# Kernel tuning notes

Measured on AMD Instinct MI355X. Metric: run time of the kernel, lower is better.

## Reference

```python
import jax, jax.numpy as jnp
import numpy as np

N_ATOMS = 8192
N_PAIRS = 65536
F = 128        # n_atombasis
R = 20         # n_radialbasis
B = 5          # graph_n_blocks
EPS = 1e-8     # stability constant


def setup_inputs() -> dict:
    key = jax.random.key(0)
    ks = jax.random.split(key, 16)
    rn = lambda k, shape, s=0.05: jax.random.normal(k, shape, dtype=jnp.float32) * s
    return {
        "features": jax.random.normal(ks[0], (N_ATOMS, F), jnp.float32),
        "distances": jax.random.uniform(ks[1], (N_PAIRS,), jnp.float32, 0.5, 5.0),
        "vectors": jax.random.normal(ks[2], (N_PAIRS, 3), jnp.float32),
        "cutoffs": jax.random.uniform(ks[3], (N_PAIRS,), jnp.float32),
        "rbfs": jax.random.normal(ks[4], (N_PAIRS, R), jnp.float32),
        "filter_W": rn(ks[5], (R, B * 3 * F)),
        "filter_b": jnp.zeros((B * 3 * F,), jnp.float32),
        "int_W1": rn(ks[6], (B, F, F)),
        "int_b1": jnp.zeros((B, F), jnp.float32),
        "int_W2": rn(ks[7], (B, F, 3 * F)),
        "int_b2": jnp.zeros((B, 3 * F), jnp.float32),
        "mix_Wv": rn(ks[8], (B, F, 2 * F)),
        "mix_W1": rn(ks[9], (B, 2 * F, F)),
        "mix_b1": jnp.zeros((B, F), jnp.float32),
        "mix_W2": rn(ks[10], (B, F, 3 * F)),
        "mix_b2": jnp.zeros((B, 3 * F), jnp.float32),
        "idx_i": jax.random.randint(ks[11], (N_PAIRS,), 0, N_ATOMS),
        "idx_j": jax.random.randint(ks[12], (N_PAIRS,), 0, N_ATOMS),
    }


def reference(features, distances, vectors, cutoffs, rbfs,
              filter_W, filter_b, int_W1, int_b1, int_W2, int_b2,
              mix_Wv, mix_W1, mix_b1, mix_W2, mix_b2, idx_i, idx_j):
    n_atoms = features.shape[0]
    # Cutoff-weighted radial filters, one (3F) chunk per block: [P, B*3F]
    descriptors = (rbfs @ filter_W + filter_b) * cutoffs[:, None]
    dir_ij = vectors / distances[:, None]                       # [P, 3]

    q = features[:, None, :]                                    # [N, 1, F]
    mu = jnp.zeros((n_atoms, 3, F), dtype=features.dtype)       # [N, 3, F]

    for b in range(B):
        # --- interaction block ---
        x = jax.nn.silu(q @ int_W1[b] + int_b1[b]) @ int_W2[b] + int_b2[b]  # [N,1,3F]
        Wij = descriptors[:, None, b * 3 * F:(b + 1) * 3 * F]               # [P,1,3F]
        xj = x[idx_j] * Wij                                                 # [P,1,3F]
        muj = mu[idx_j]                                                     # [P,3,F]
        dq, dmuR, dmumu = jnp.split(xj, 3, axis=-1)                         # [P,1,F] each
        dmu = dmuR * dir_ij[:, :, None] + dmumu * muj                       # [P,3,F]
        q = q + jax.ops.segment_sum(dq, idx_i, num_segments=n_atoms)
        mu = mu + jax.ops.segment_sum(dmu, idx_i, num_segments=n_atoms)

        # --- mixing block ---
        mu_V, mu_W = jnp.split(mu @ mix_Wv[b], 2, axis=-1)                  # [N,3,F] each
        mu_Vn = jnp.sqrt(jnp.sum(mu_V ** 2, axis=-2, keepdims=True) + EPS)  # [N,1,F]
        ctx = jnp.concatenate([q, mu_Vn], axis=-1)                          # [N,1,2F]
        y = jax.nn.silu(ctx @ mix_W1[b] + mix_b1[b]) @ mix_W2[b] + mix_b2[b]
        dq_i, dmu_i, dqmu_i = jnp.split(y, 3, axis=-1)                      # [N,1,F] each
        q = q + dq_i + dqmu_i * jnp.sum(mu_V * mu_W, axis=1, keepdims=True)
        mu = mu + dmu_i * mu_W

    return q[:, 0, :], mu
```

## Files before the change

kernel.cpp:

```cpp
#include <hip/hip_runtime.h>
#include <hip/hip_bf16.h>

#define NA 8192
#define NP 65536
#define WROW 1920
#define CAP 40

typedef short short8 __attribute__((ext_vector_type(8)));
typedef short short4v __attribute__((ext_vector_type(4)));
typedef float floatx4 __attribute__((ext_vector_type(4)));

static __device__ __forceinline__ short f2bf(float f) {
    union { float f; unsigned u; } v; v.f = f;
    unsigned r = v.u + 0x7FFF + ((v.u >> 16) & 1);
    return (short)(r >> 16);
}
static __device__ __forceinline__ float bf2f(short s) {
    union { unsigned u; float f; } v;
    v.u = ((unsigned)(unsigned short)s) << 16;
    return v.f;
}
static __device__ __forceinline__ unsigned char f2fp8(float f) {
    int p = __builtin_amdgcn_cvt_pk_fp8_f32(f, 0.f, 0, false);
    return (unsigned char)(p & 0xFF);
}
static __device__ __forceinline__ float fp82f(unsigned char b) {
    return __builtin_amdgcn_cvt_f32_fp8((int)b, 0);
}
static __device__ __forceinline__ float silu(float v) {
    return v / (1.f + __expf(-v));
}

static __device__ __forceinline__ void swz(const float* __restrict__ src,
                                           short* __restrict__ dst,
                                           int K, int N, int idx) {
    int kn = K * N;
    int b = idx / kn;
    int r = idx - b * kn;
    int tile = r >> 9, li = r & 511;
    int lane = li >> 3, bb = li & 7;
    int Kt = K >> 5;
    int nt = tile / Kt, kt = tile - nt * Kt;
    int k = kt * 32 + (lane >> 4) * 8 + bb;
    int n = nt * 16 + (lane & 15);
    dst[idx] = f2bf(src[b * kn + k * N + n]);
}

__global__ __launch_bounds__(256) void k_setup(const float* __restrict__ iW1,
                                               const float* __restrict__ iW2,
                                               const float* __restrict__ mWv,
                                               const float* __restrict__ mW1,
                                               const float* __restrict__ mW2,
                                               const float* __restrict__ fW,
                                               short* __restrict__ W1t,
                                               short* __restrict__ W2t,
                                               short* __restrict__ Wvt,
                                               short* __restrict__ mW1t,
                                               short* __restrict__ mW2t,
                                               short* __restrict__ fWt,
                                               const float* __restrict__ feat,
                                               float* __restrict__ q,
                                               short* __restrict__ q_bf) {
    int idx = blockIdx.x * 256 + threadIdx.x;
    if (idx < 962560) {
        if (idx < 81920)       { swz(iW1, W1t, 128, 128, idx); return; }
        idx -= 81920;
        if (idx < 245760)      { swz(iW2, W2t, 128, 384, idx); return; }
        idx -= 245760;
        if (idx < 163840)      { swz(mWv, Wvt, 128, 256, idx); return; }
        idx -= 163840;
        if (idx < 163840)      { swz(mW1, mW1t, 256, 128, idx); return; }
        idx -= 163840;
        if (idx < 245760)      { swz(mW2, mW2t, 128, 384, idx); return; }
        idx -= 245760;
        {
            int b = idx / 12288;
            int r = idx - b * 12288;
            int nt = r >> 9;
            int li = r & 511;
            int lane = li >> 3, bb = li & 7;
            int k = (lane >> 4) * 8 + bb;
            int n = nt * 16 + (lane & 15);
            fWt[b * 12288 + r] = (k < 20) ? f2bf(fW[k * WROW + b * 384 + n]) : (short)0;
        }
        return;
    }
    idx -= 962560;
    if (idx < NA * 128) { float v = feat[idx]; q[idx] = v; q_bf[idx] = f2bf(v); }
}

__global__ __launch_bounds__(256) void k_fillprep(const int* __restrict__ idx_i,
                                                  const int* __restrict__ idx_j,
                                                  int* __restrict__ cursor,
                                                  const float* __restrict__ cut,
                                                  const float* __restrict__ dist,
                                                  const float* __restrict__ vec,
                                                  const float* __restrict__ rbfs,
                                                  float* __restrict__ cut_csr,
                                                  float4* __restrict__ dirj,
                                                  short* __restrict__ rbf_c) {
    int p = blockIdx.x * 256 + threadIdx.x;
    if (p >= NP) return;
    int i = idx_i[p];
    int pos = atomicAdd(&cursor[i], 1);
    if (pos >= CAP) return;
    int e = i * CAP + pos;
    float c = cut[p];
    cut_csr[e] = c;
    float invd = 1.f / dist[p];
    float4 d;
    d.x = vec[p * 3 + 0] * invd;
    d.y = vec[p * 3 + 1] * invd;
    d.z = vec[p * 3 + 2] * invd;
    d.w = __int_as_float(idx_j[p]);
    dirj[e] = d;
    #pragma unroll
    for (int k = 0; k < 20; ++k) rbf_c[e * 32 + k] = f2bf(rbfs[p * 20 + k] * c);
    #pragma unroll
    for (int k = 20; k < 32; ++k) rbf_c[e * 32 + k] = 0;
}

__global__ __launch_bounds__(256) void k_x(const short* __restrict__ q_bf,
                                           const short* __restrict__ W1sw,
                                           const short* __restrict__ W2sw,
                                           const float* __restrict__ b1,
                                           const float* __restrict__ b2,
                                           unsigned char* __restrict__ xarr) {
    __shared__ __align__(16) short qtile[16 * 136];
    __shared__ __align__(16) short hs[16 * 136];
    int t = threadIdx.x;
    int wv = t >> 6, lane = t & 63, quad = lane >> 4, l16 = lane & 15;
    int a0 = blockIdx.x * 16;

    #pragma unroll
    for (int it = 0; it < 2; ++it) {
        int c = it * 256 + t;
        int row = c >> 5, col4 = c & 31;
        *(short4v*)(qtile + row * 136 + col4 * 4) =
            *(const short4v*)(q_bf + (a0 + row) * 128 + col4 * 4);
    }
    __syncthreads();

    floatx4 acc0 = {0.f, 0.f, 0.f, 0.f}, acc1 = {0.f, 0.f, 0.f, 0.f};
    #pragma unroll
    for (int kk = 0; kk < 4; ++kk) {
        short8 a  = *(const short8*)(qtile + l16 * 136 + kk * 32 + quad * 8);
        short8 b0 = *(const short8*)(W1sw + ((wv * 2 + 0) * 4 + kk) * 512 + lane * 8);
        short8 bq = *(const short8*)(W1sw + ((wv * 2 + 1) * 4 + kk) * 512 + lane * 8);
        acc0 = __builtin_amdgcn_mfma_f32_16x16x32_bf16(a, b0, acc0, 0, 0, 0);
        acc1 = __builtin_amdgcn_mfma_f32_16x16x32_bf16(a, bq, acc1, 0, 0, 0);
    }
    __syncthreads();
    {
        int n0 = wv * 32 + l16;
        float bia0 = b1[n0], bia1 = b1[n0 + 16];
        #pragma unroll
        for (int r = 0; r < 4; ++r) {
            int m = quad * 4 + r;
            hs[m * 136 + n0]      = f2bf(silu(acc0[r] + bia0));
            hs[m * 136 + n0 + 16] = f2bf(silu(acc1[r] + bia1));
        }
    }
    __syncthreads();
    floatx4 acc[6];
    #pragma unroll
    for (int jj = 0; jj < 6; ++jj) acc[jj] = {0.f, 0.f, 0.f, 0.f};
    #pragma unroll
    for (int kk = 0; kk < 4; ++kk) {
        short8 a = *(const short8*)(hs + l16 * 136 + kk * 32 + quad * 8);
        #pragma unroll
        for (int jj = 0; jj < 6; ++jj) {
            short8 b = *(const short8*)(W2sw + ((wv * 6 + jj) * 4 + kk) * 512 + lane * 8);
            acc[jj] = __builtin_amdgcn_mfma_f32_16x16x32_bf16(a, b, acc[jj], 0, 0, 0);
        }
    }
    #pragma unroll
    for (int jj = 0; jj < 6; ++jj) {
        int n = wv * 96 + jj * 16 + l16;
        float bia = b2[n];
        #pragma unroll
        for (int r = 0; r < 4; ++r) {
            int m = quad * 4 + r;
            xarr[(size_t)((a0 + m) * 128 + (n & 127)) * 4 + (n >> 7)] =
                f2fp8(acc[jj][r] + bia);
        }
    }
}

__global__ __launch_bounds__(256, 4) void k_gather(const unsigned* __restrict__ xarr_r,
                                                   const uint2* __restrict__ muarr_r,
                                                   const short* __restrict__ rbf_c,
                                                   const short* __restrict__ fWt,
                                                   const float* __restrict__ fbp,
                                                   const float4* __restrict__ dirj,
                                                   const float* __restrict__ cut_csr,
                                                   const int* __restrict__ cursor,
                                                   short* __restrict__ dqg,
                                                   short* __restrict__ dmug) {
    __shared__ short dlds[16 * 392];
    __shared__ float pm[3 * 512];
    int i = blockIdx.x;
    int t = threadIdx.x;
    int wv = t >> 6, lane = t & 63, quad = lane >> 4, l16 = lane & 15;
    int start = i * CAP;
    int f0 = lane * 2;

    float4 dj[4];
    #pragma unroll
    for (int m = 0; m < 4; ++m) dj[m] = dirj[start + wv + 4 * m];
    short8 afrag = *(const short8*)(rbf_c + (size_t)(start + l16) * 32 + quad * 8);
    float cc[4];
    #pragma unroll
    for (int r = 0; r < 4; ++r) cc[r] = cut_csr[start + quad * 4 + r];

    int cnt = cursor[i];
    if (cnt > CAP) cnt = CAP;
    int end = start + cnt;

    float acc[8];
    #pragma unroll
    for (int k = 0; k < 8; ++k) acc[k] = 0.f;

    for (int e0 = start; e0 < end; e0 += 16) {
        if (e0 > start) {
            __syncthreads();
            #pragma unroll
            for (int m = 0; m < 4; ++m) dj[m] = dirj[e0 + wv + 4 * m];
            afrag = *(const short8*)(rbf_c + (size_t)(e0 + l16) * 32 + quad * 8);
            #pragma unroll
            for (int r = 0; r < 4; ++r) cc[r] = cut_csr[e0 + quad * 4 + r];
        }
        int clen = end - e0; if (clen > 16) clen = 16;
        #pragma unroll
        for (int nt = 0; nt < 6; ++nt) {
            int col = wv * 96 + nt * 16 + l16;
            short8 bfr = *(const short8*)(fWt + (wv * 6 + nt) * 512 + lane * 8);
            floatx4 z = {0.f, 0.f, 0.f, 0.f};
            floatx4 ad = __builtin_amdgcn_mfma_f32_16x16x32_bf16(afrag, bfr, z, 0, 0, 0);
            float fbv = fbp[col];
            dlds[(quad * 4 + 0) * 392 + col] = f2bf(ad[0] + fbv * cc[0]);
            dlds[(quad * 4 + 1) * 392 + col] = f2bf(ad[1] + fbv * cc[1]);
            dlds[(quad * 4 + 2) * 392 + col] = f2bf(ad[2] + fbv * cc[2]);
            dlds[(quad * 4 + 3) * 392 + col] = f2bf(ad[3] + fbv * cc[3]);
        }
        uint2 xr[4]; uint4 mr[4];
        #pragma unroll
        for (int m = 0; m < 4; ++m) {
            int le = wv + 4 * m;
            int j = (le < clen) ? __float_as_int(dj[m].w) : 0;
            xr[m] = *(const uint2*)(xarr_r + (size_t)j * 128 + f0);
            mr[m] = *(const uint4*)(muarr_r + (size_t)j * 128 + f0);
        }
        __syncthreads();
        #pragma unroll
        for (int m = 0; m < 4; ++m) {
            int le = wv + 4 * m;
            if (le < clen) {
                unsigned wa = *(const unsigned*)(dlds + le * 392 + f0);
                unsigned wb = *(const unsigned*)(dlds + le * 392 + 128 + f0);
                unsigned wc = *(const unsigned*)(dlds + le * 392 + 256 + f0);
                float wa0 = bf2f((short)(wa & 0xFFFF)), wa1 = bf2f((short)(wa >> 16));
                float wb0 = bf2f((short)(wb & 0xFFFF)), wb1 = bf2f((short)(wb >> 16));
                float wc0 = bf2f((short)(wc & 0xFFFF)), wc1 = bf2f((short)(wc >> 16));
                {
                    unsigned xw = xr[m].x;
                    float x0 = fp82f((unsigned char)(xw & 0xFF));
                    float x1 = fp82f((unsigned char)((xw >> 8) & 0xFF));
                    float x2 = fp82f((unsigned char)((xw >> 16) & 0xFF));
                    float u0 = bf2f((short)(mr[m].x & 0xFFFF));
                    float u1 = bf2f((short)(mr[m].x >> 16));
                    float u2 = bf2f((short)(mr[m].y & 0xFFFF));
                    acc[0] += x0 * wa0;
                    float xb = x1 * wb0, xc = x2 * wc0;
                    acc[1] += xb * dj[m].x + xc * u0;
                    acc[2] += xb * dj[m].y + xc * u1;
                    acc[3] += xb * dj[m].z + xc * u2;
                }
                {
                    unsigned xw = xr[m].y;
                    float x0 = fp82f((unsigned char)(xw & 0xFF));
                    float x1 = fp82f((unsigned char)((xw >> 8) & 0xFF));
                    float x2 = fp82f((unsigned char)((xw >> 16) & 0xFF));
                    float u0 = bf2f((short)(mr[m].z & 0xFFFF));
                    float u1 = bf2f((short)(mr[m].z >> 16));
                    float u2 = bf2f((short)(mr[m].w & 0xFFFF));
                    acc[4] += x0 * wa1;
                    float xb = x1 * wb1, xc = x2 * wc1;
                    acc[5] += xb * dj[m].x + xc * u0;
                    acc[6] += xb * dj[m].y + xc * u1;
                    acc[7] += xb * dj[m].z + xc * u2;
                }
            }
        }
    }
    if (wv) {
        float* p = pm + (wv - 1) * 512;
        #pragma unroll
        for (int arr = 0; arr < 4; ++arr) {
            float2 v; v.x = acc[arr]; v.y = acc[arr + 4];
            *(float2*)(p + arr * 128 + f0) = v;
        }
    }
    __syncthreads();
    if (wv == 0) {
        #pragma unroll
        for (int arr = 0; arr < 4; ++arr) {
            float2 p0 = *(const float2*)(pm + 0 * 512 + arr * 128 + f0);
            float2 p1 = *(const float2*)(pm + 1 * 512 + arr * 128 + f0);
            float2 p2 = *(const float2*)(pm + 2 * 512 + arr * 128 + f0);
            float sl = acc[arr]     + p0.x + p1.x + p2.x;
            float sh = acc[arr + 4] + p0.y + p1.y + p2.y;
            unsigned o = (unsigned)(unsigned short)f2bf(sl) |
                         ((unsigned)(unsigned short)f2bf(sh) << 16);
            if (arr == 0) *(unsigned*)(dqg + i * 128 + f0) = o;
            else          *(unsigned*)(dmug + (i * 3 + arr - 1) * 128 + f0) = o;
        }
    }
}

__global__ __launch_bounds__(512, 4) void k_mixx(const float* __restrict__ mu_ro,
                                                 const short* __restrict__ dmug,
                                                 const float* __restrict__ q_ro,
                                                 const short* __restrict__ dqg,
                                                 const short* __restrict__ Wvsw,
                                                 const short* __restrict__ W1sw,
                                                 const short* __restrict__ W2sw,
                                                 const float* __restrict__ b1,
                                                 const float* __restrict__ b2,
                                                 float* __restrict__ q,
                                                 float* __restrict__ mu,
                                                 unsigned* __restrict__ xarr_w,
                                                 uint2* __restrict__ muarr_w,
                                                 const short* __restrict__ xW1sw,
                                                 const short* __restrict__ xW2sw,
                                                 const float* __restrict__ xb1,
                                                 const float* __restrict__ xb2,
                                                 int do_x) {
    __shared__ __align__(16) char smem[51968];
    short* ms    = (short*)(smem);
    short* qtile = (short*)(smem + 13056);
    short* Vv    = (short*)(smem + 17408);
    short* hs    = (short*)(smem + 17408);
    short* Vw    = (short*)(smem + 30464);
    short* vnb   = (short*)(smem + 43520);
    short* sb    = (short*)(smem + 47872);
    unsigned char* xls = (unsigned char*)(smem + 43520);
    int t = threadIdx.x;
    int wv = t >> 6, lane = t & 63, quad = lane >> 4, l16 = lane & 15;
    int a0 = blockIdx.x * 16;
    int co = wv * 16 + l16;

    float qnf[4];
    float mnf[4][3];
    #pragma unroll
    for (int r = 0; r < 4; ++r) {
        int m = quad * 4 + r;
        int ga = a0 + m;
        int gq = ga * 128 + co;
        qnf[r] = q_ro[gq] + bf2f(dqg[gq]);
        qtile[m * 136 + co] = f2bf(qnf[r]);
        #pragma unroll
        for (int d = 0; d < 3; ++d) {
            int gm = (ga * 3 + d) * 128 + co;
            mnf[r][d] = mu_ro[gm] + bf2f(dmug[gm]);
            ms[(m * 3 + d) * 136 + co] = f2bf(mnf[r][d]);
        }
    }
    __syncthreads();

    {
        floatx4 acc[3][2];
        #pragma unroll
        for (int mt = 0; mt < 3; ++mt)
            #pragma unroll
            for (int nt = 0; nt < 2; ++nt) acc[mt][nt] = {0.f, 0.f, 0.f, 0.f};
        #pragma unroll
        for (int kk = 0; kk < 4; ++kk) {
            short8 a[3];
            #pragma unroll
            for (int mt = 0; mt < 3; ++mt)
                a[mt] = *(const short8*)(ms + (mt * 16 + l16) * 136 + kk * 32 + quad * 8);
            #pragma unroll
            for (int nt = 0; nt < 2; ++nt) {
                short8 b = *(const short8*)(Wvsw + ((wv * 2 + nt) * 4 + kk) * 512 + lane * 8);
                #pragma unroll
                for (int mt = 0; mt < 3; ++mt)
                    acc[mt][nt] = __builtin_amdgcn_mfma_f32_16x16x32_bf16(a[mt], b, acc[mt][nt], 0, 0, 0);
            }
        }
        #pragma unroll
        for (int mt = 0; mt < 3; ++mt)
            #pragma unroll
            for (int nt = 0; nt < 2; ++nt)
                #pragma unroll
                for (int r = 0; r < 4; ++r) {
                    int row = mt * 16 + quad * 4 + r;
                    int col = wv * 32 + nt * 16 + l16;
                    short v = f2bf(acc[mt][nt][r]);
                    if (col < 128) Vv[row * 136 + col] = v;
                    else           Vw[row * 136 + col - 128] = v;
                }
    }
    __syncthreads();
    #pragma unroll
    for (int k = 0; k < 4; ++k) {
        int idx = k * 512 + t;
        int a = idx >> 7, c = idx & 127;
        float v0 = bf2f(Vv[(a * 3 + 0) * 136 + c]);
        float v1 = bf2f(Vv[(a * 3 + 1) * 136 + c]);
        float v2 = bf2f(Vv[(a * 3 + 2) * 136 + c]);
        float w0 = bf2f(Vw[(a * 3 + 0) * 136 + c]);
        float w1 = bf2f(Vw[(a * 3 + 1) * 136 + c]);
        float w2 = bf2f(Vw[(a * 3 + 2) * 136 + c]);
        vnb[a * 136 + c] = f2bf(sqrtf(v0 * v0 + v1 * v1 + v2 * v2 + 1e-8f));
        sb[a * 128 + c]  = f2bf(v0 * w0 + v1 * w1 + v2 * w2);
    }
    __syncthreads();
    {
        floatx4 accq = {0.f, 0.f, 0.f, 0.f};
        floatx4 accv = {0.f, 0.f, 0.f, 0.f};
        #pragma unroll
        for (int kk = 0; kk < 4; ++kk) {
            short8 aq = *(const short8*)(qtile + l16 * 136 + kk * 32 + quad * 8);
            short8 av = *(const short8*)(vnb + l16 * 136 + kk * 32 + quad * 8);
            short8 bq = *(const short8*)(W1sw + (wv * 8 + kk) * 512 + lane * 8);
            short8 bv = *(const short8*)(W1sw + (wv * 8 + 4 + kk) * 512 + lane * 8);
            accq = __builtin_amdgcn_mfma_f32_16x16x32_bf16(aq, bq, accq, 0, 0, 0);
            accv = __builtin_amdgcn_mfma_f32_16x16x32_bf16(av, bv, accv, 0, 0, 0);
        }
        int n0 = wv * 16 + l16;
        float bia0 = b1[n0];
        #pragma unroll
        for (int r = 0; r < 4; ++r) {
            int m = quad * 4 + r;
            hs[m * 136 + n0] = f2bf(silu(accq[r] + accv[r] + bia0));
        }
    }
    __syncthreads();
    {
        floatx4 accB[3];
        #pragma unroll
        for (int c = 0; c < 3; ++c) accB[c] = {0.f, 0.f, 0.f, 0.f};
        #pragma unroll
        for (int kk = 0; kk < 4; ++kk) {
            short8 a = *(const short8*)(hs + l16 * 136 + kk * 32 + quad * 8);
            #pragma unroll
            for (int c = 0; c < 3; ++c) {
                short8 b = *(const short8*)(W2sw + ((c * 8 + wv) * 4 + kk) * 512 + lane * 8);
                accB[c] = __builtin_amdgcn_mfma_f32_16x16x32_bf16(a, b, accB[c], 0, 0, 0);
            }
        }
        float bq_  = b2[co];
        float bm_  = b2[128 + co];
        float bqm_ = b2[256 + co];
        #pragma unroll
        for (int r = 0; r < 4; ++r) {
            int m = quad * 4 + r;
            int ga = a0 + m;
            float dq   = accB[0][r] + bq_;
            float dmu  = accB[1][r] + bm_;
            float dqmu = accB[2][r] + bqm_;
            float sv = bf2f(sb[m * 128 + co]);
            int gq = ga * 128 + co;
            float qn = qnf[r] + dq + dqmu * sv;
            q[gq] = qn;
            qtile[m * 136 + co] = f2bf(qn);
            float mn[3];
            #pragma unroll
            for (int d = 0; d < 3; ++d) {
                int gm = (ga * 3 + d) * 128 + co;
                float mw = bf2f(Vw[(m * 3 + d) * 136 + co]);
                mn[d] = mnf[r][d] + dmu * mw;
                mu[gm] = mn[d];
            }
            if (do_x) {
                uint2 mw2;
                mw2.x = (unsigned)(unsigned short)f2bf(mn[0]) |
                        ((unsigned)(unsigned short)f2bf(mn[1]) << 16);
                mw2.y = (unsigned)(unsigned short)f2bf(mn[2]);
                muarr_w[gq] = mw2;
            }
        }
    }
    if (!do_x) return;
    __syncthreads();
    {
        floatx4 acc0 = {0.f, 0.f, 0.f, 0.f};
        #pragma unroll
        for (int kk = 0; kk < 4; ++kk) {
            short8 a  = *(const short8*)(qtile + l16 * 136 + kk * 32 + quad * 8);
            short8 b0 = *(const short8*)(xW1sw + (wv * 4 + kk) * 512 + lane * 8);
            acc0 = __builtin_amdgcn_mfma_f32_16x16x32_bf16(a, b0, acc0, 0, 0, 0);
        }
        int n0 = wv * 16 + l16;
        float bia0 = xb1[n0];
        #pragma unroll
        for (int r = 0; r < 4; ++r) {
            int m = quad * 4 + r;
            hs[m * 136 + n0] = f2bf(silu(acc0[r] + bia0));
        }
    }
    __syncthreads();
    {
        floatx4 acc[3];
        #pragma unroll
        for (int jj = 0; jj < 3; ++jj) acc[jj] = {0.f, 0.f, 0.f, 0.f};
        #pragma unroll
        for (int kk = 0; kk < 4; ++kk) {
            short8 a = *(const short8*)(hs + l16 * 136 + kk * 32 + quad * 8);
            #pragma unroll
            for (int jj = 0; jj < 3; ++jj) {
                short8 b = *(const short8*)(xW2sw + ((wv * 3 + jj) * 4 + kk) * 512 + lane * 8);
                acc[jj] = __builtin_amdgcn_mfma_f32_16x16x32_bf16(a, b, acc[jj], 0, 0, 0);
            }
        }
        #pragma unroll
        for (int jj = 0; jj < 3; ++jj) {
            int n = wv * 48 + jj * 16 + l16;
            float bia = xb2[n];
            #pragma unroll
            for (int r = 0; r < 4; ++r) {
                int m = quad * 4 + r;
                xls[(m * 128 + (n & 127)) * 4 + (n >> 7)] = f2fp8(acc[jj][r] + bia);
            }
        }
    }
    __syncthreads();
    {
        const unsigned* xlsu = (const unsigned*)xls;
        unsigned* xw = xarr_w + (size_t)a0 * 128;
        #pragma unroll
        for (int k = 0; k < 4; ++k) {
            int idx = k * 512 + t;
            xw[idx] = xlsu[idx];
        }
    }
}

extern "C" void kernel_launch(void* const* d_in, const int* in_sizes, int n_in,
                              void* d_out, int out_size, void* d_ws, size_t ws_size,
                              hipStream_t stream) {
    const float* feat = (const float*)d_in[0];
    const float* dist = (const float*)d_in[1];
    const float* vec  = (const float*)d_in[2];
    const float* cut  = (const float*)d_in[3];
    const float* rbfs = (const float*)d_in[4];
    const float* fW   = (const float*)d_in[5];
    const float* fb   = (const float*)d_in[6];
    const float* iW1  = (const float*)d_in[7];
    const float* ib1  = (const float*)d_in[8];
    const float* iW2  = (const float*)d_in[9];
    const float* ib2  = (const float*)d_in[10];
    const float* mWv  = (const float*)d_in[11];
    const float* mW1  = (const float*)d_in[12];
    const float* mb1  = (const float*)d_in[13];
    const float* mW2  = (const float*)d_in[14];
    const float* mb2  = (const float*)d_in[15];
    const int* idx_i  = (const int*)d_in[16];
    const int* idx_j  = (const int*)d_in[17];

    float* q  = (float*)d_out;
    float* mu = (float*)d_out + NA * 128;

    char* w = (char*)d_ws;
    unsigned* xarr0  = (unsigned*)(w);
    unsigned* xarr1  = (unsigned*)(w + 4194304);
    uint2*    muarr0 = (uint2*)(w + 8388608);
    uint2*    muarr1 = (uint2*)(w + 16777216);
    short* dqg     = (short*)(w + 25165824);
    short* dmug    = (short*)(w + 27262976);
    short* q_bf    = (short*)(w + 33554432);
    short* W1t     = (short*)(w + 35651584);
    short* W2t     = (short*)(w + 35815424);
    short* Wvt     = (short*)(w + 36306944);
    short* mW1t    = (short*)(w + 36634624);
    short* mW2t    = (short*)(w + 36962304);
    short* fWt     = (short*)(w + 37453824);
    int*   cursor  = (int*)(w + 37576704);
    float4* dirj   = (float4*)(w + 37609472);
    float* cut_csr = (float*)(w + 42852608);
    short* rbf_c   = (short*)(w + 44163392);

    hipMemsetAsync(cursor, 0, NA * 4, stream);
    hipMemsetAsync(muarr0, 0, NA * 128 * 8, stream);
    hipMemsetAsync(mu, 0, (size_t)NA * 384 * 4, stream);

    k_setup<<<7856, 256, 0, stream>>>(iW1, iW2, mWv, mW1, mW2, fW,
                                      W1t, W2t, Wvt, mW1t, mW2t, fWt,
                                      feat, q, q_bf);
    k_fillprep<<<NP / 256, 256, 0, stream>>>(idx_i, idx_j, cursor, cut, dist, vec,
                                             rbfs, cut_csr, dirj, rbf_c);

    k_x<<<NA / 16, 256, 0, stream>>>(q_bf, W1t, W2t, ib1, ib2, (unsigned char*)xarr0);
    unsigned* xa[2] = {xarr0, xarr1};
    uint2*    ma[2] = {muarr0, muarr1};
    for (int b = 0; b < 5; ++b) {
        int bn = (b + 1) % 5;
        k_gather<<<NA, 256, 0, stream>>>(xa[b & 1], ma[b & 1], rbf_c, fWt + b * 12288,
                                         fb + b * 384, dirj, cut_csr, cursor,
                                         dqg, dmug);
        k_mixx<<<NA / 16, 512, 0, stream>>>(mu, dmug, q, dqg,
                                            Wvt + b * 32768,
                                            mW1t + b * 32768, mW2t + b * 49152,
                                            mb1 + b * 128, mb2 + b * 384,
                                            q, mu,
                                            xa[(b + 1) & 1], ma[(b + 1) & 1],
                                            W1t + bn * 16384, W2t + bn * 49152,
                                            ib1 + bn * 128, ib2 + bn * 384,
                                            (b < 4) ? 1 : 0);
    }
}
```

Baseline: 398.5 us.

## Store x and mu gather arrays as padding-free planar planes; fold memsets into setup

Result: faster. 356.3 us (median of 2 runs) (-10.6%).

```diff
diff --git a/kernel.cpp b/kernel.cpp
--- a/kernel.cpp
+++ b/kernel.cpp
@@ -5,6 +5,7 @@
 #define NP 65536
 #define WROW 1920
 #define CAP 40
+#define PLANE 1048576
 
 typedef short short8 __attribute__((ext_vector_type(8)));
 typedef short short4v __attribute__((ext_vector_type(4)));
@@ -60,7 +61,10 @@
                                                short* __restrict__ fWt,
                                                const float* __restrict__ feat,
                                                float* __restrict__ q,
-                                               short* __restrict__ q_bf) {
+                                               float* __restrict__ mu,
+                                               short* __restrict__ q_bf,
+                                               unsigned short* __restrict__ mp0,
+                                               int* __restrict__ cursor) {
     int idx = blockIdx.x * 256 + threadIdx.x;
     if (idx < 962560) {
         if (idx < 81920)       { swz(iW1, W1t, 128, 128, idx); return; }
@@ -87,6 +91,9 @@
     }
     idx -= 962560;
     if (idx < NA * 128) { float v = feat[idx]; q[idx] = v; q_bf[idx] = f2bf(v); }
+    mu[idx] = 0.f;
+    mp0[idx] = 0;
+    if (idx < NA) cursor[idx] = 0;
 }
 
 __global__ __launch_bounds__(256) void k_fillprep(const int* __restrict__ idx_i,
@@ -125,7 +132,7 @@
                                            const short* __restrict__ W2sw,
                                            const float* __restrict__ b1,
                                            const float* __restrict__ b2,
-                                           unsigned char* __restrict__ xarr) {
+                                           unsigned char* __restrict__ xp) {
     __shared__ __align__(16) short qtile[16 * 136];
     __shared__ __align__(16) short hs[16 * 136];
     int t = threadIdx.x;
@@ -181,14 +188,14 @@
         #pragma unroll
         for (int r = 0; r < 4; ++r) {
             int m = quad * 4 + r;
-            xarr[(size_t)((a0 + m) * 128 + (n & 127)) * 4 + (n >> 7)] =
+            xp[(size_t)(n >> 7) * PLANE + (size_t)(a0 + m) * 128 + (n & 127)] =
                 f2fp8(acc[jj][r] + bia);
         }
     }
 }
 
-__global__ __launch_bounds__(256, 4) void k_gather(const unsigned* __restrict__ xarr_r,
-                                                   const uint2* __restrict__ muarr_r,
+__global__ __launch_bounds__(256, 4) void k_gather(const unsigned char* __restrict__ xp_r,
+                                                   const unsigned short* __restrict__ mp_r,
                                                    const short* __restrict__ rbf_c,
                                                    const short* __restrict__ fWt,
                                                    const float* __restrict__ fbp,
@@ -243,13 +250,19 @@
             dlds[(quad * 4 + 2) * 392 + col] = f2bf(ad[2] + fbv * cc[2]);
             dlds[(quad * 4 + 3) * 392 + col] = f2bf(ad[3] + fbv * cc[3]);
         }
-        uint2 xr[4]; uint4 mr[4];
+        unsigned short xr0[4], xr1[4], xr2[4];
+        unsigned mr0[4], mr1[4], mr2[4];
         #pragma unroll
         for (int m = 0; m < 4; ++m) {
             int le = wv + 4 * m;
             int j = (le < clen) ? __float_as_int(dj[m].w) : 0;
-            xr[m] = *(const uint2*)(xarr_r + (size_t)j * 128 + f0);
-            mr[m] = *(const uint4*)(muarr_r + (size_t)j * 128 + f0);
+            size_t bx = (size_t)j * 128 + f0;
+            xr0[m] = *(const unsigned short*)(xp_r + bx);
+            xr1[m] = *(const unsigned short*)(xp_r + PLANE + bx);
+            xr2[m] = *(const unsigned short*)(xp_r + 2 * PLANE + bx);
+            mr0[m] = *(const unsigned*)(mp_r + bx);
+            mr1[m] = *(const unsigned*)(mp_r + PLANE + bx);
+            mr2[m] = *(const unsigned*)(mp_r + 2 * PLANE + bx);
         }
         __syncthreads();
         #pragma unroll
@@ -263,13 +276,12 @@
                 float wb0 = bf2f((short)(wb & 0xFFFF)), wb1 = bf2f((short)(wb >> 16));
                 float wc0 = bf2f((short)(wc & 0xFFFF)), wc1 = bf2f((short)(wc >> 16));
                 {
-                    unsigned xw = xr[m].x;
-                    float x0 = fp82f((unsigned char)(xw & 0xFF));
-                    float x1 = fp82f((unsigned char)((xw >> 8) & 0xFF));
-                    float x2 = fp82f((unsigned char)((xw >> 16) & 0xFF));
-                    float u0 = bf2f((short)(mr[m].x & 0xFFFF));
-                    float u1 = bf2f((short)(mr[m].x >> 16));
-                    float u2 = bf2f((short)(mr[m].y & 0xFFFF));
+                    float x0 = fp82f((unsigned char)(xr0[m] & 0xFF));
+                    float x1 = fp82f((unsigned char)(xr1[m] & 0xFF));
+                    float x2 = fp82f((unsigned char)(xr2[m] & 0xFF));
+                    float u0 = bf2f((short)(mr0[m] & 0xFFFF));
+                    float u1 = bf2f((short)(mr1[m] & 0xFFFF));
+                    float u2 = bf2f((short)(mr2[m] & 0xFFFF));
                     acc[0] += x0 * wa0;
                     float xb = x1 * wb0, xc = x2 * wc0;
                     acc[1] += xb * dj[m].x + xc * u0;
@@ -277,13 +289,12 @@
                     acc[3] += xb * dj[m].z + xc * u2;
                 }
                 {
-                    unsigned xw = xr[m].y;
-                    float x0 = fp82f((unsigned char)(xw & 0xFF));
-                    float x1 = fp82f((unsigned char)((xw >> 8) & 0xFF));
-                    float x2 = fp82f((unsigned char)((xw >> 16) & 0xFF));
-                    float u0 = bf2f((short)(mr[m].z & 0xFFFF));
-                    float u1 = bf2f((short)(mr[m].z >> 16));
-                    float u2 = bf2f((short)(mr[m].w & 0xFFFF));
+                    float x0 = fp82f((unsigned char)(xr0[m] >> 8));
+                    float x1 = fp82f((unsigned char)(xr1[m] >> 8));
+                    float x2 = fp82f((unsigned char)(xr2[m] >> 8));
+                    float u0 = bf2f((short)(mr0[m] >> 16));
+                    float u1 = bf2f((short)(mr1[m] >> 16));
+                    float u2 = bf2f((short)(mr2[m] >> 16));
                     acc[4] += x0 * wa1;
                     float xb = x1 * wb1, xc = x2 * wc1;
                     acc[5] += xb * dj[m].x + xc * u0;
@@ -329,8 +340,8 @@
                                                  const float* __restrict__ b2,
                                                  float* __restrict__ q,
                                                  float* __restrict__ mu,
-                                                 unsigned* __restrict__ xarr_w,
-                                                 uint2* __restrict__ muarr_w,
+                                                 unsigned char* __restrict__ xp_w,
+                                                 unsigned short* __restrict__ mp_w,
                                                  const short* __restrict__ xW1sw,
                                                  const short* __restrict__ xW2sw,
                                                  const float* __restrict__ xb1,
@@ -474,11 +485,9 @@
                 mu[gm] = mn[d];
             }
             if (do_x) {
-                uint2 mw2;
-                mw2.x = (unsigned)(unsigned short)f2bf(mn[0]) |
-                        ((unsigned)(unsigned short)f2bf(mn[1]) << 16);
-                mw2.y = (unsigned)(unsigned short)f2bf(mn[2]);
-                muarr_w[gq] = mw2;
+                mp_w[(size_t)0 * PLANE + gq] = (unsigned short)f2bf(mn[0]);
+                mp_w[(size_t)1 * PLANE + gq] = (unsigned short)f2bf(mn[1]);
+                mp_w[(size_t)2 * PLANE + gq] = (unsigned short)f2bf(mn[2]);
             }
         }
     }
@@ -521,18 +530,19 @@
             #pragma unroll
             for (int r = 0; r < 4; ++r) {
                 int m = quad * 4 + r;
-                xls[(m * 128 + (n & 127)) * 4 + (n >> 7)] = f2fp8(acc[jj][r] + bia);
+                xls[(n >> 7) * 2048 + m * 128 + (n & 127)] = f2fp8(acc[jj][r] + bia);
             }
         }
     }
     __syncthreads();
     {
         const unsigned* xlsu = (const unsigned*)xls;
-        unsigned* xw = xarr_w + (size_t)a0 * 128;
-        #pragma unroll
-        for (int k = 0; k < 4; ++k) {
+        #pragma unroll
+        for (int k = 0; k < 3; ++k) {
             int idx = k * 512 + t;
-            xw[idx] = xlsu[idx];
+            int p = idx >> 9;
+            int wo = idx & 511;
+            *(unsigned*)(xp_w + (size_t)p * PLANE + (size_t)a0 * 128 + wo * 4) = xlsu[idx];
         }
     }
 }
@@ -563,37 +573,33 @@
     float* mu = (float*)d_out + NA * 128;
 
     char* w = (char*)d_ws;
-    unsigned* xarr0  = (unsigned*)(w);
-    unsigned* xarr1  = (unsigned*)(w + 4194304);
-    uint2*    muarr0 = (uint2*)(w + 8388608);
-    uint2*    muarr1 = (uint2*)(w + 16777216);
-    short* dqg     = (short*)(w + 25165824);
-    short* dmug    = (short*)(w + 27262976);
-    short* q_bf    = (short*)(w + 33554432);
-    short* W1t     = (short*)(w + 35651584);
-    short* W2t     = (short*)(w + 35815424);
-    short* Wvt     = (short*)(w + 36306944);
-    short* mW1t    = (short*)(w + 36634624);
-    short* mW2t    = (short*)(w + 36962304);
-    short* fWt     = (short*)(w + 37453824);
-    int*   cursor  = (int*)(w + 37576704);
-    float4* dirj   = (float4*)(w + 37609472);
-    float* cut_csr = (float*)(w + 42852608);
-    short* rbf_c   = (short*)(w + 44163392);
-
-    hipMemsetAsync(cursor, 0, NA * 4, stream);
-    hipMemsetAsync(muarr0, 0, NA * 128 * 8, stream);
-    hipMemsetAsync(mu, 0, (size_t)NA * 384 * 4, stream);
-
-    k_setup<<<7856, 256, 0, stream>>>(iW1, iW2, mWv, mW1, mW2, fW,
-                                      W1t, W2t, Wvt, mW1t, mW2t, fWt,
-                                      feat, q, q_bf);
+    unsigned char*  xp0 = (unsigned char*)(w);
+    unsigned char*  xp1 = (unsigned char*)(w + 3145728);
+    unsigned short* mp0 = (unsigned short*)(w + 6291456);
+    unsigned short* mp1 = (unsigned short*)(w + 12582912);
+    short* dqg     = (short*)(w + 18874368);
+    short* dmug    = (short*)(w + 20971520);
+    short* q_bf    = (short*)(w + 27262976);
+    short* W1t     = (short*)(w + 29360128);
+    short* W2t     = (short*)(w + 29523968);
+    short* Wvt     = (short*)(w + 30015488);
+    short* mW1t    = (short*)(w + 30343168);
+    short* mW2t    = (short*)(w + 30670848);
+    short* fWt     = (short*)(w + 31162368);
+    int*   cursor  = (int*)(w + 31285248);
+    float4* dirj   = (float4*)(w + 31318016);
+    float* cut_csr = (float*)(w + 36561152);
+    short* rbf_c   = (short*)(w + 37871936);
+
+    k_setup<<<16048, 256, 0, stream>>>(iW1, iW2, mWv, mW1, mW2, fW,
+                                       W1t, W2t, Wvt, mW1t, mW2t, fWt,
+                                       feat, q, mu, q_bf, mp0, cursor);
     k_fillprep<<<NP / 256, 256, 0, stream>>>(idx_i, idx_j, cursor, cut, dist, vec,
                                              rbfs, cut_csr, dirj, rbf_c);
 
-    k_x<<<NA / 16, 256, 0, stream>>>(q_bf, W1t, W2t, ib1, ib2, (unsigned char*)xarr0);
-    unsigned* xa[2] = {xarr0, xarr1};
-    uint2*    ma[2] = {muarr0, muarr1};
+    k_x<<<NA / 16, 256, 0, stream>>>(q_bf, W1t, W2t, ib1, ib2, xp0);
+    unsigned char*  xa[2] = {xp0, xp1};
+    unsigned short* ma[2] = {mp0, mp1};
     for (int b = 0; b < 5; ++b) {
         int bn = (b + 1) % 5;
         k_gather<<<NA, 256, 0, stream>>>(xa[b & 1], ma[b & 1], rbf_c, fWt + b * 12288,
```
